# Kernel optimization log

Hardware: AMD Instinct MI355X
Metric: run time of the kernel (lower is better)

The kernel has to match this reference:

```python
import jax, jax.numpy as jnp
import numpy as np
from jax import lax

D_MODEL = 1024
D_STATE = 16
D_CONV = 4
EXPAND = 2
D_INNER = EXPAND * D_MODEL
LN_EPS = 1e-5


def setup_inputs() -> dict:
    key = jax.random.key(0)
    ks = jax.random.split(key, 12)
    B, L = 4, 1024
    s = lambda fan_in: 1.0 / np.sqrt(fan_in)
    inp = {
        "x": jax.random.normal(ks[0], (B, L, D_MODEL), jnp.float32),
        # in_proj: d_model -> 2*d_inner (stored as (in, out))
        "W_in": jax.random.normal(ks[1], (D_MODEL, 2 * D_INNER), jnp.float32) * s(D_MODEL),
        "b_in": jnp.zeros((2 * D_INNER,), jnp.float32),
        # depthwise causal conv1d, kernel (d_inner, 1, d_conv)
        "conv_w": jax.random.normal(ks[2], (D_INNER, 1, D_CONV), jnp.float32) * s(D_CONV),
        "conv_b": jnp.zeros((D_INNER,), jnp.float32),
        # x_proj: d_inner -> 2*d_state
        "W_xp": jax.random.normal(ks[3], (D_INNER, 2 * D_STATE), jnp.float32) * s(D_INNER),
        "b_xp": jnp.zeros((2 * D_STATE,), jnp.float32),
        # dt_proj: d_inner -> d_inner
        "W_dt": jax.random.normal(ks[4], (D_INNER, D_INNER), jnp.float32) * s(D_INNER),
        "b_dt": jnp.zeros((D_INNER,), jnp.float32),
        # A_log = log(arange(1, d_state+1)) repeated over d_inner
        "A_log": jnp.log(jnp.broadcast_to(jnp.arange(1, D_STATE + 1, dtype=jnp.float32), (D_INNER, D_STATE))),
        "D_param": jnp.ones((D_INNER,), jnp.float32),
        # out_proj: d_inner -> d_model
        "W_out": jax.random.normal(ks[5], (D_INNER, D_MODEL), jnp.float32) * s(D_INNER),
        "b_out": jnp.zeros((D_MODEL,), jnp.float32),
        "ln_g": jnp.ones((D_MODEL,), jnp.float32),
        "ln_b": jnp.zeros((D_MODEL,), jnp.float32),
    }
    return inp


def _causal_depthwise_conv(x, w, b):
    # x: (B, d_inner, L); w: (d_inner, 1, d_conv). Left-pad d_conv-1 => causal.
    y = lax.conv_general_dilated(
        x, w, window_strides=(1,), padding=[(D_CONV - 1, 0)],
        dimension_numbers=("NCH", "OIH", "NCH"), feature_group_count=D_INNER)
    return y + b[None, :, None]


def _ssm(x, A, Bm, Cm, dt, D_param):
    # x, dt: (B,L,D)  A: (D,N)  Bm, Cm: (B,L,N)
    A_disc = jnp.exp(dt[..., None] * A)               # (B,L,D,N)
    dBx = (dt * x)[..., None] * Bm[:, :, None, :]     # (B,L,D,N) = dt*B*x_t
    h0 = jnp.zeros(x.shape[:1] + A.shape, x.dtype)    # (B,D,N)

    def step(h, inputs):
        a, bx, c = inputs                              # (B,D,N),(B,D,N),(B,N)
        h = a * h + bx
        y = jnp.einsum("bdn,bn->bd", h, c)
        return h, y

    _, ys = lax.scan(step, h0, (jnp.swapaxes(A_disc, 0, 1),
                                jnp.swapaxes(dBx, 0, 1),
                                jnp.swapaxes(Cm, 0, 1)))
    y = jnp.swapaxes(ys, 0, 1)                         # (B,L,D)
    return y + x * D_param


def reference(x, W_in, b_in, conv_w, conv_b, W_xp, b_xp, W_dt, b_dt,
              A_log, D_param, W_out, b_out, ln_g, ln_b):
    residual = x
    xr = x @ W_in + b_in                               # (B,L,2*d_inner)
    xi, res = jnp.split(xr, 2, axis=-1)
    xi = jax.nn.silu(xi)
    xi = jnp.swapaxes(xi, 1, 2)                        # (B,d_inner,L)
    xi = _causal_depthwise_conv(xi, conv_w, conv_b)
    xi = jnp.swapaxes(xi, 1, 2)
    xi = jax.nn.silu(xi)
    bc = xi @ W_xp + b_xp                              # (B,L,2*d_state)
    Bm, Cm = jnp.split(bc, 2, axis=-1)
    dt = jax.nn.softplus(xi @ W_dt + b_dt)
    A = -jnp.exp(A_log)                                # (d_inner, d_state)
    y = _ssm(xi, A, Bm, Cm, dt, D_param)
    y = y * jax.nn.silu(res)
    out = y @ W_out + b_out
    z = out + residual
    mu = jnp.mean(z, axis=-1, keepdims=True)
    var = jnp.var(z, axis=-1, keepdims=True)
    return (z - mu) * jax.lax.rsqrt(var + LN_EPS) * ln_g + ln_b
```

## Files before the change

kernel.cpp:

```cpp
#include <hip/hip_runtime.h>
#include <math.h>

#define D_MODEL 1024
#define D_INNER 2048
#define D_STATE 16
#define D_CONV  4
#define NCHUNK  32
#define LCHUNK  32

typedef unsigned short u16;
typedef __attribute__((ext_vector_type(8))) short short8;
typedef __attribute__((ext_vector_type(4))) float f32x4;
typedef __attribute__((ext_vector_type(4))) unsigned short u16x4;
typedef __attribute__((ext_vector_type(8))) unsigned short u16x8;

__device__ __forceinline__ float silu_f(float x) { return x / (1.f + __expf(-x)); }
__device__ __forceinline__ float softplus_f(float x) {
    return fmaxf(x, 0.f) + log1pf(__expf(-fabsf(x)));
}
__device__ __forceinline__ u16 f2bf(float f) {
    union { float f; unsigned u; } c; c.f = f;
    unsigned r = c.u + 0x7fffu + ((c.u >> 16) & 1u);
    return (u16)(r >> 16);
}
__device__ __forceinline__ float bf2f(u16 v) {
    union { unsigned u; float f; } c; c.u = ((unsigned)v) << 16; return c.f;
}
__device__ __forceinline__ void gload_lds16(const void* g, void* l) {
    __builtin_amdgcn_global_load_lds((const __attribute__((address_space(1))) void*)g,
                                     (__attribute__((address_space(3))) void*)l, 16, 0, 0);
}

__global__ __launch_bounds__(256)
void f32_to_bf16_kernel(const float* __restrict__ in, u16* __restrict__ out, int n4)
{
    const int i = blockIdx.x * 256 + threadIdx.x;
    if (i >= n4) return;
    const float4 v = *(const float4*)&in[(size_t)i * 4];
    u16x4 o; o.x = f2bf(v.x); o.y = f2bf(v.y); o.z = f2bf(v.z); o.w = f2bf(v.w);
    *(u16x4*)&out[(size_t)i * 4] = o;
}

__global__ __launch_bounds__(256)
void transpose_bf16_kernel(const float* __restrict__ W, u16* __restrict__ Wt, int K, int N)
{
    __shared__ float tile[32][33];
    const int tx = threadIdx.x & 31, ty = threadIdx.x >> 5;
    const int n0 = blockIdx.x * 32, k0 = blockIdx.y * 32;
#pragma unroll
    for (int q = 0; q < 4; q++)
        tile[ty + q * 8][tx] = W[(size_t)(k0 + ty + q * 8) * N + n0 + tx];
    __syncthreads();
#pragma unroll
    for (int q = 0; q < 4; q++)
        Wt[(size_t)(n0 + ty + q * 8) * K + k0 + tx] = f2bf(tile[tx][ty + q * 8]);
}

template <int MODE>
__global__ __launch_bounds__(512, 2)
void gemm_mfma256(const u16* __restrict__ A, const u16* __restrict__ Bt,
                  const float* __restrict__ bias,
                  void* __restrict__ out0v, void* __restrict__ out1v,
                  int M, int N, int K)
{
    __shared__ __align__(16) short As[2][256 * 64];
    __shared__ __align__(16) short Bs[2][256 * 64];

    const int tid = threadIdx.x;
    const int wid = tid >> 6, lane = tid & 63;
    const int wr = wid >> 2, wc = wid & 3;
    const int row0 = blockIdx.y * 256, col0 = blockIdx.x * 256;
    const int kg = lane >> 4, r16 = lane & 15;

    f32x4 acc[8][4] = {};

    const u16* Abase = A + (size_t)row0 * K;
    const u16* Bbase = Bt + (size_t)col0 * K;

#define STAGE_A(bi, kk) do {                                                    \
        _Pragma("unroll")                                                       \
        for (int q = 0; q < 4; q++) {                                           \
            const int c = (q << 9) + tid;                                       \
            const int r = c >> 3;                                               \
            const int ks8 = (((c & 7) ^ (r & 7)) << 3);                         \
            gload_lds16(Abase + (size_t)r * K + (kk) + ks8,                     \
                        &As[bi][((q << 9) + (wid << 6)) << 3]);                 \
        }                                                                       \
    } while (0)
#define STAGE_B(bi, kk) do {                                                    \
        _Pragma("unroll")                                                       \
        for (int q = 0; q < 4; q++) {                                           \
            const int c = (q << 9) + tid;                                       \
            const int r = c >> 3;                                               \
            const int ks8 = (((c & 7) ^ (r & 7)) << 3);                         \
            gload_lds16(Bbase + (size_t)r * K + (kk) + ks8,                     \
                        &Bs[bi][((q << 9) + (wid << 6)) << 3]);                 \
        }                                                                       \
    } while (0)

    const int nt = K >> 6;
    STAGE_A(0, 0);
    STAGE_B(0, 0);

    int cur = 0;
    const int rx = r16 & 7;
    for (int t = 0; t < nt; ++t) {
        if (t + 1 < nt) {
            STAGE_A(cur ^ 1, (t + 1) << 6);
            asm volatile("s_waitcnt vmcnt(4)" ::: "memory");
        } else {
            asm volatile("s_waitcnt vmcnt(0)" ::: "memory");
        }
        __builtin_amdgcn_s_barrier();

#pragma unroll
        for (int ks = 0; ks < 2; ks++) {
            const int sl8 = (((ks << 2) + kg) ^ rx) << 3;
            short8 af[8], bg[4];
#pragma unroll
            for (int i = 0; i < 8; i++) {
                const int r = wr * 128 + i * 16 + r16;
                af[i] = *(const short8*)&As[cur][r * 64 + sl8];
            }
#pragma unroll
            for (int j = 0; j < 4; j++) {
                const int r = wc * 64 + j * 16 + r16;
                bg[j] = *(const short8*)&Bs[cur][r * 64 + sl8];
            }
            __builtin_amdgcn_s_setprio(1);
#pragma unroll
            for (int i = 0; i < 8; i++)
#pragma unroll
                for (int j = 0; j < 4; j++)
                    acc[i][j] = __builtin_amdgcn_mfma_f32_16x16x32_bf16(af[i], bg[j], acc[i][j], 0, 0, 0);
            __builtin_amdgcn_s_setprio(0);
            if (ks == 0 && t + 1 < nt)
                STAGE_B(cur ^ 1, (t + 1) << 6);
        }

        asm volatile("s_waitcnt lgkmcnt(0)" ::: "memory");
        __builtin_amdgcn_s_barrier();
        cur ^= 1;
    }
#undef STAGE_A
#undef STAGE_B

#pragma unroll
    for (int i = 0; i < 8; i++) {
#pragma unroll
        for (int j = 0; j < 4; j++) {
#pragma unroll
            for (int r = 0; r < 4; r++) {
                const int row = row0 + wr * 128 + i * 16 + kg * 4 + r;
                const int col = col0 + wc * 64 + j * 16 + r16;
                float v = acc[i][j][r] + bias[col];
                if (MODE == 0) {
                    u16* o0 = (u16*)out0v; u16* o1 = (u16*)out1v;
                    if (col < D_INNER) o0[(size_t)row * D_INNER + col] = f2bf(silu_f(v));
                    else               o1[(size_t)row * D_INNER + (col - D_INNER)] = f2bf(v);
                } else {
                    ((float*)out0v)[(size_t)row * N + col] = softplus_f(v);
                }
            }
        }
    }
}

template <int MODE>
__global__ __launch_bounds__(256)
void gemm_mfma_128(const u16* __restrict__ A, const u16* __restrict__ Bt,
                   const float* __restrict__ bias, const float* __restrict__ aux,
                   float* __restrict__ out0, int M, int N, int K)
{
    __shared__ __align__(16) short As[3][4096];
    __shared__ __align__(16) short Bs[3][4096];

    const int tid = threadIdx.x;
    const int wid = tid >> 6, lane = tid & 63;
    const int wr = wid >> 1, wc = wid & 1;
    const int row0 = blockIdx.y * 128, col0 = blockIdx.x * 128;

    f32x4 acc[4][4] = {};

    const int c0 = wid * 128 + lane;
    const int c1 = c0 + 64;
    const u16* Abase = A + (size_t)row0 * K;
    const u16* Bbase = Bt + (size_t)col0 * K;

    const int gsl8 = (((lane & 3) ^ ((lane >> 3) & 3)) << 3);
    const int kg = lane >> 4, r16 = lane & 15;
    const int sl8 = ((kg ^ ((r16 >> 1) & 3)) << 3);

#define STAGE(bi, kk) do {                                                                   \
        gload_lds16(Abase + (size_t)(c0 >> 2) * K + (kk) + gsl8, &As[bi][wid * 1024]);       \
        gload_lds16(Abase + (size_t)(c1 >> 2) * K + (kk) + gsl8, &As[bi][wid * 1024 + 512]); \
        gload_lds16(Bbase + (size_t)(c0 >> 2) * K + (kk) + gsl8, &Bs[bi][wid * 1024]);       \
        gload_lds16(Bbase + (size_t)(c1 >> 2) * K + (kk) + gsl8, &Bs[bi][wid * 1024 + 512]); \
    } while (0)

    const int nt = K >> 5;
    STAGE(0, 0);
    STAGE(1, 32);
    int cs = 0;
    for (int t = 0; t < nt; ++t) {
        if (t + 2 < nt) {
            const int ss = (cs + 2 >= 3) ? cs - 1 : cs + 2;
            STAGE(ss, (t + 2) << 5);
            asm volatile("s_waitcnt vmcnt(8)" ::: "memory");
        } else if (t + 1 < nt) {
            asm volatile("s_waitcnt vmcnt(4)" ::: "memory");
        } else {
            asm volatile("s_waitcnt vmcnt(0)" ::: "memory");
        }
        __builtin_amdgcn_s_barrier();

        short8 af[4], bg[4];
#pragma unroll
        for (int i = 0; i < 4; i++) {
            const int r = wr * 64 + i * 16 + r16;
            af[i] = *(const short8*)&As[cs][r * 32 + sl8];
        }
#pragma unroll
        for (int j = 0; j < 4; j++) {
            const int r = wc * 64 + j * 16 + r16;
            bg[j] = *(const short8*)&Bs[cs][r * 32 + sl8];
        }
        __builtin_amdgcn_s_setprio(1);
#pragma unroll
        for (int i = 0; i < 4; i++)
#pragma unroll
            for (int j = 0; j < 4; j++)
                acc[i][j] = __builtin_amdgcn_mfma_f32_16x16x32_bf16(af[i], bg[j], acc[i][j], 0, 0, 0);
        __builtin_amdgcn_s_setprio(0);

        asm volatile("s_waitcnt lgkmcnt(0)" ::: "memory");
        __builtin_amdgcn_s_barrier();
        cs = (cs + 1 >= 3) ? 0 : cs + 1;
    }
#undef STAGE

#pragma unroll
    for (int i = 0; i < 4; i++) {
#pragma unroll
        for (int j = 0; j < 4; j++) {
#pragma unroll
            for (int r = 0; r < 4; r++) {
                const int row = row0 + wr * 64 + i * 16 + kg * 4 + r;
                const int col = col0 + wc * 64 + j * 16 + r16;
                float v = acc[i][j][r] + bias[col];
                if (MODE == 1) out0[(size_t)row * N + col] = softplus_f(v);
                else           out0[(size_t)row * N + col] = v + aux[(size_t)row * N + col];
            }
        }
    }
}

__global__ __launch_bounds__(256)
void conv_silu8_kernel(const u16* __restrict__ xi, const float* __restrict__ w,
                       const float* __restrict__ cb, u16* __restrict__ xcb, int total8)
{
    const int i = blockIdx.x * 256 + threadIdx.x;
    if (i >= total8) return;
    const size_t i8 = (size_t)i * 8;
    const int d8 = (int)(i8 & (D_INNER - 1));
    const int l = (int)((i8 >> 11) & 1023);

    float acc[8];
#pragma unroll
    for (int c = 0; c < 8; c++) acc[c] = cb[d8 + c];

    float4 wv[8];
#pragma unroll
    for (int c = 0; c < 8; c++) wv[c] = *(const float4*)&w[(d8 + c) * 4];

#pragma unroll
    for (int k = 0; k < D_CONV; k++) {
        if (l + k - (D_CONV - 1) >= 0) {
            const u16x8 v = *(const u16x8*)&xi[i8 + (size_t)(k - (D_CONV - 1)) * D_INNER];
            const float wk0 = ((const float*)&wv[0])[k];
#pragma unroll
            for (int c = 0; c < 8; c++) {
                const float wk = ((const float*)&wv[c])[k];
                acc[c] = fmaf(wk, bf2f(v[c]), acc[c]);
            }
            (void)wk0;
        }
    }
    u16x8 o;
#pragma unroll
    for (int c = 0; c < 8; c++) o[c] = f2bf(silu_f(acc[c]));
    *(u16x8*)&xcb[i8] = o;
}

__global__ __launch_bounds__(256)
void xproj_mfma_kernel(const u16* __restrict__ A, const u16* __restrict__ Wt,
                       const float* __restrict__ bxp, float* __restrict__ bc)
{
    const int wid = threadIdx.x >> 6, lane = threadIdx.x & 63;
    const int kg = lane >> 4, r16 = lane & 15;
    const int tok0 = blockIdx.x * 64 + wid * 16;

    f32x4 acc[2] = {};
#pragma unroll 4
    for (int k0 = 0; k0 < D_INNER; k0 += 32) {
        const short8 a  = *(const short8*)&A[(size_t)(tok0 + r16) * D_INNER + k0 + kg * 8];
        const short8 b0 = *(const short8*)&Wt[(size_t)r16 * D_INNER + k0 + kg * 8];
        const short8 b1 = *(const short8*)&Wt[(size_t)(16 + r16) * D_INNER + k0 + kg * 8];
        acc[0] = __builtin_amdgcn_mfma_f32_16x16x32_bf16(a, b0, acc[0], 0, 0, 0);
        acc[1] = __builtin_amdgcn_mfma_f32_16x16x32_bf16(a, b1, acc[1], 0, 0, 0);
    }
#pragma unroll
    for (int j = 0; j < 2; j++)
#pragma unroll
        for (int r = 0; r < 4; r++) {
            const int token = tok0 + kg * 4 + r;
            const int c = j * 16 + r16;
            bc[(size_t)token * 32 + c] = acc[j][r] + bxp[c];
        }
}

__global__ __launch_bounds__(256)
void ssm_s1_kernel(const u16* __restrict__ xcbf, const float* __restrict__ dt,
                   const float* __restrict__ bc, const float* __restrict__ A_log,
                   float* __restrict__ hend, float* __restrict__ dtsum)
{
    const int tid = threadIdx.x;
    const int d = blockIdx.x * 256 + tid;
    const int c = blockIdx.y;
    const int b = blockIdx.z;

    __shared__ float sB[LCHUNK][16];
    {
        if (tid < LCHUNK * 4) {
            const int row = tid >> 2, c4 = (tid & 3) << 2;
            *(float4*)&sB[row][c4] = *(const float4*)&bc[((size_t)(b * 1024 + c * LCHUNK + row)) * 32 + c4];
        }
    }

    float Aln[D_STATE];
#pragma unroll
    for (int q = 0; q < 4; q++) {
        const f32x4 a = *(const f32x4*)&A_log[(size_t)d * D_STATE + q * 4];
        Aln[q * 4 + 0] = -__expf(a.x); Aln[q * 4 + 1] = -__expf(a.y);
        Aln[q * 4 + 2] = -__expf(a.z); Aln[q * 4 + 3] = -__expf(a.w);
    }

    const size_t base = ((size_t)(b * 1024 + c * LCHUNK)) * D_INNER + d;
    const float* dtp = dt + base;
    const u16* xp = xcbf + base;

    float h[D_STATE] = {};
    float S = 0.f;
    __syncthreads();

#pragma unroll 16
    for (int j = 0; j < LCHUNK; j++) {
        const float dtf = dtp[(size_t)j * D_INNER];
        const float xf = bf2f(xp[(size_t)j * D_INNER]);
        const float dtx = dtf * xf;
        S += dtf;
#pragma unroll
        for (int n = 0; n < D_STATE; n++) {
            const float a = __expf(dtf * Aln[n]);
            h[n] = fmaf(a, h[n], dtx * sB[j][n]);
        }
    }

    const size_t ob = ((size_t)(b * NCHUNK + c) * D_INNER + d);
#pragma unroll
    for (int q = 0; q < 4; q++) {
        f32x4 hv = {h[q * 4 + 0], h[q * 4 + 1], h[q * 4 + 2], h[q * 4 + 3]};
        *(f32x4*)&hend[ob * D_STATE + q * 4] = hv;
    }
    dtsum[ob] = S;
}

__global__ __launch_bounds__(256)
void ssm_s2_kernel(const float* __restrict__ hend, const float* __restrict__ dtsum,
                   const float* __restrict__ A_log, float* __restrict__ hin)
{
    const int tid = threadIdx.x;
    const int d = blockIdx.x * 16 + (tid >> 4);
    const int n = tid & 15;
    const int b = blockIdx.y;

    const float Aln = -__expf(A_log[(size_t)d * D_STATE + n]);
    float h = 0.f;
#pragma unroll
    for (int c = 0; c < NCHUNK; c++) {
        const size_t ob = ((size_t)(b * NCHUNK + c) * D_INNER + d);
        hin[ob * D_STATE + n] = h;
        const float P = __expf(Aln * dtsum[ob]);
        h = fmaf(P, h, hend[ob * D_STATE + n]);
    }
}

__global__ __launch_bounds__(256)
void ssm_s3_kernel(const u16* __restrict__ xcbf, const float* __restrict__ dt,
                   const float* __restrict__ bc, const float* __restrict__ A_log,
                   const float* __restrict__ Dp, const u16* __restrict__ resbf,
                   const float* __restrict__ hin, u16* __restrict__ ybf)
{
    const int tid = threadIdx.x;
    const int d = blockIdx.x * 256 + tid;
    const int c = blockIdx.y;
    const int b = blockIdx.z;

    __shared__ float sbc[LCHUNK][32];
    {
        const int row = tid >> 3, c4 = (tid & 7) << 2;
        if (row < LCHUNK)
            *(float4*)&sbc[row][c4] = *(const float4*)&bc[((size_t)(b * 1024 + c * LCHUNK + row)) * 32 + c4];
    }

    float Aln[D_STATE];
#pragma unroll
    for (int q = 0; q < 4; q++) {
        const f32x4 a = *(const f32x4*)&A_log[(size_t)d * D_STATE + q * 4];
        Aln[q * 4 + 0] = -__expf(a.x); Aln[q * 4 + 1] = -__expf(a.y);
        Aln[q * 4 + 2] = -__expf(a.z); Aln[q * 4 + 3] = -__expf(a.w);
    }
    const float Dv = Dp[d];

    float h[D_STATE];
    const size_t ob = ((size_t)(b * NCHUNK + c) * D_INNER + d);
#pragma unroll
    for (int q = 0; q < 4; q++) {
        const f32x4 hv = *(const f32x4*)&hin[ob * D_STATE + q * 4];
        h[q * 4 + 0] = hv.x; h[q * 4 + 1] = hv.y; h[q * 4 + 2] = hv.z; h[q * 4 + 3] = hv.w;
    }

    const size_t base = ((size_t)(b * 1024 + c * LCHUNK)) * D_INNER + d;
    const float* dtp = dt + base;
    const u16* xp = xcbf + base;
    const u16* rp = resbf + base;
    u16* yp = ybf + base;

    __syncthreads();

#pragma unroll 16
    for (int j = 0; j < LCHUNK; j++) {
        const float dtf = dtp[(size_t)j * D_INNER];
        const float xf = bf2f(xp[(size_t)j * D_INNER]);
        const float rf = bf2f(rp[(size_t)j * D_INNER]);
        const float dtx = dtf * xf;
        float yv = 0.f;
#pragma unroll
        for (int n = 0; n < D_STATE; n++) {
            const float a = __expf(dtf * Aln[n]);
            h[n] = fmaf(a, h[n], dtx * sbc[j][n]);
            yv = fmaf(h[n], sbc[j][16 + n], yv);
        }
        yv = (yv + xf * Dv) * silu_f(rf);
        yp[(size_t)j * D_INNER] = f2bf(yv);
    }
}

__global__ __launch_bounds__(256)
void layernorm_kernel(const float* __restrict__ z, const float* __restrict__ g,
                      const float* __restrict__ beta, float* __restrict__ out)
{
    const int row = blockIdx.x;
    const int tid = threadIdx.x;
    const float* zr = z + (size_t)row * D_MODEL;
    const float4 v = *(const float4*)&zr[tid << 2];
    float s = v.x + v.y + v.z + v.w;
    float ss = v.x * v.x + v.y * v.y + v.z * v.z + v.w * v.w;

    __shared__ float sm[256], sq[256];
    sm[tid] = s; sq[tid] = ss;
    __syncthreads();
    for (int off = 128; off > 0; off >>= 1) {
        if (tid < off) { sm[tid] += sm[tid + off]; sq[tid] += sq[tid + off]; }
        __syncthreads();
    }
    const float mean = sm[0] * (1.f / D_MODEL);
    const float var = sq[0] * (1.f / D_MODEL) - mean * mean;
    const float rstd = rsqrtf(var + 1e-5f);

    float4 o;
    o.x = (v.x - mean) * rstd * g[(tid << 2) + 0] + beta[(tid << 2) + 0];
    o.y = (v.y - mean) * rstd * g[(tid << 2) + 1] + beta[(tid << 2) + 1];
    o.z = (v.z - mean) * rstd * g[(tid << 2) + 2] + beta[(tid << 2) + 2];
    o.w = (v.w - mean) * rstd * g[(tid << 2) + 3] + beta[(tid << 2) + 3];
    *(float4*)&out[(size_t)row * D_MODEL + (tid << 2)] = o;
}

extern "C" void kernel_launch(void* const* d_in, const int* in_sizes, int n_in,
                              void* d_out, int out_size, void* d_ws, size_t ws_size,
                              hipStream_t stream)
{
    const float* x      = (const float*)d_in[0];
    const float* W_in   = (const float*)d_in[1];
    const float* b_in   = (const float*)d_in[2];
    const float* conv_w = (const float*)d_in[3];
    const float* conv_b = (const float*)d_in[4];
    const float* W_xp   = (const float*)d_in[5];
    const float* b_xp   = (const float*)d_in[6];
    const float* W_dt   = (const float*)d_in[7];
    const float* b_dt   = (const float*)d_in[8];
    const float* A_log  = (const float*)d_in[9];
    const float* D_par  = (const float*)d_in[10];
    const float* W_out  = (const float*)d_in[11];
    const float* b_out  = (const float*)d_in[12];
    const float* ln_g   = (const float*)d_in[13];
    const float* ln_b   = (const float*)d_in[14];
    float* out = (float*)d_out;

    const int BL = in_sizes[0] / D_MODEL;
    const int Bb = BL / 1024;
    const size_t BLD = (size_t)BL * D_INNER;

    float* ws    = (float*)d_ws;
    float* dtb   = ws;
    float* bcbuf = dtb + BLD;
    float* hend  = bcbuf + (size_t)BL * 32;
    float* dtsum = hend + (size_t)Bb * NCHUNK * D_INNER * D_STATE;
    float* hinb  = dtsum + (size_t)Bb * NCHUNK * D_INNER;
    u16*   xibf  = (u16*)(hinb + (size_t)Bb * NCHUNK * D_INNER * D_STATE);
    u16*   resbf = xibf + BLD;
    u16*   xcbf  = resbf + BLD;
    u16*   xbf   = xcbf + BLD;
    u16*   wxpT  = xbf + (size_t)BL * D_MODEL;
    u16*   wtmp  = wxpT + 32 * D_INNER;
    u16*   ybf   = xibf;
    float* zbuf  = dtb;

    f32_to_bf16_kernel<<<(BL * D_MODEL / 4 + 255) / 256, 256, 0, stream>>>(x, xbf, BL * D_MODEL / 4);

    transpose_bf16_kernel<<<dim3(2 * D_INNER / 32, D_MODEL / 32), 256, 0, stream>>>(W_in, wtmp, D_MODEL, 2 * D_INNER);

    gemm_mfma256<0><<<dim3(2 * D_INNER / 256, BL / 256), 512, 0, stream>>>(
        xbf, wtmp, b_in, xibf, resbf, BL, 2 * D_INNER, D_MODEL);

    transpose_bf16_kernel<<<dim3(1, D_INNER / 32), 256, 0, stream>>>(W_xp, wxpT, D_INNER, 32);

    conv_silu8_kernel<<<(int)(BLD / 8 / 256), 256, 0, stream>>>(
        xibf, conv_w, conv_b, xcbf, (int)(BLD / 8));

    xproj_mfma_kernel<<<BL / 64, 256, 0, stream>>>(xcbf, wxpT, b_xp, bcbuf);

    transpose_bf16_kernel<<<dim3(D_INNER / 32, D_INNER / 32), 256, 0, stream>>>(W_dt, wtmp, D_INNER, D_INNER);

    gemm_mfma_128<1><<<dim3(D_INNER / 128, BL / 128), 256, 0, stream>>>(
        xcbf, wtmp, b_dt, nullptr, dtb, BL, D_INNER, D_INNER);

    ssm_s1_kernel<<<dim3(D_INNER / 256, NCHUNK, Bb), 256, 0, stream>>>(
        xcbf, dtb, bcbuf, A_log, hend, dtsum);

    ssm_s2_kernel<<<dim3(D_INNER / 16, Bb), 256, 0, stream>>>(
        hend, dtsum, A_log, hinb);

    ssm_s3_kernel<<<dim3(D_INNER / 256, NCHUNK, Bb), 256, 0, stream>>>(
        xcbf, dtb, bcbuf, A_log, D_par, resbf, hinb, ybf);

    transpose_bf16_kernel<<<dim3(D_MODEL / 32, D_INNER / 32), 256, 0, stream>>>(W_out, wtmp, D_INNER, D_MODEL);

    gemm_mfma_128<2><<<dim3(D_MODEL / 128, BL / 128), 256, 0, stream>>>(
        ybf, wtmp, b_out, x, zbuf, BL, D_MODEL, D_INNER);

    layernorm_kernel<<<BL, 256, 0, stream>>>(zbuf, ln_g, ln_b, out);
}
```

Before: 327.9 us.

## Store dt as bf16 and add a 256x128 double-buffered dt-projection GEMM

Replaces the 128x128 GEMM for the dt projection with a new 512-thread, 256x128-tile kernel. It uses an XOR-swizzled double-buffered LDS layout, staggers A and B prefetches around the MFMA work, and writes softplus(dt) as bf16 instead of fp32. Both SSM scan kernels now read dt as bf16, which halves dt traffic on the write and on both read passes. The workspace is relaid out so the out-projection result reuses the chunk-state buffer. The cost is reduced dt precision feeding the exponentials in the recurrence.

```diff
diff --git a/kernel.cpp b/kernel.cpp
--- a/kernel.cpp
+++ b/kernel.cpp
@@ -166,7 +166,108 @@
     }
 }
 
-template <int MODE>
+__global__ __launch_bounds__(512, 2)
+void gemm_dt256(const u16* __restrict__ A, const u16* __restrict__ Bt,
+                const float* __restrict__ bias, u16* __restrict__ out0,
+                int M, int N, int K)
+{
+    __shared__ __align__(16) short As[2][256 * 64];
+    __shared__ __align__(16) short Bs[2][128 * 64];
+
+    const int tid = threadIdx.x;
+    const int wid = tid >> 6, lane = tid & 63;
+    const int wr = wid >> 1, wc = wid & 1;
+    const int row0 = blockIdx.y * 256, col0 = blockIdx.x * 128;
+    const int kg = lane >> 4, r16 = lane & 15;
+
+    f32x4 acc[4][4] = {};
+
+    const u16* Abase = A + (size_t)row0 * K;
+    const u16* Bbase = Bt + (size_t)col0 * K;
+
+#define STAGE_A(bi, kk) do {                                                    \
+        _Pragma("unroll")                                                       \
+        for (int q = 0; q < 4; q++) {                                           \
+            const int c = (q << 9) + tid;                                       \
+            const int r = c >> 3;                                               \
+            const int ks8 = (((c & 7) ^ (r & 7)) << 3);                         \
+            gload_lds16(Abase + (size_t)r * K + (kk) + ks8,                     \
+                        &As[bi][((q << 9) + (wid << 6)) << 3]);                 \
+        }                                                                       \
+    } while (0)
+#define STAGE_B(bi, kk) do {                                                    \
+        _Pragma("unroll")                                                       \
+        for (int q = 0; q < 2; q++) {                                           \
+            const int c = (q << 9) + tid;                                       \
+            const int r = c >> 3;                                               \
+            const int ks8 = (((c & 7) ^ (r & 7)) << 3);                         \
+            gload_lds16(Bbase + (size_t)r * K + (kk) + ks8,                     \
+                        &Bs[bi][((q << 9) + (wid << 6)) << 3]);                 \
+        }                                                                       \
+    } while (0)
+
+    const int nt = K >> 6;
+    STAGE_A(0, 0);
+    STAGE_B(0, 0);
+
+    int cur = 0;
+    const int rx = r16 & 7;
+    for (int t = 0; t < nt; ++t) {
+        if (t + 1 < nt) {
+            STAGE_A(cur ^ 1, (t + 1) << 6);
+            asm volatile("s_waitcnt vmcnt(4)" ::: "memory");
+        } else {
+            asm volatile("s_waitcnt vmcnt(0)" ::: "memory");
+        }
+        __builtin_amdgcn_s_barrier();
+
+#pragma unroll
+        for (int ks = 0; ks < 2; ks++) {
+            const int sl8 = (((ks << 2) + kg) ^ rx) << 3;
+            short8 af[4], bg[4];
+#pragma unroll
+            for (int i = 0; i < 4; i++) {
+                const int r = wr * 64 + i * 16 + r16;
+                af[i] = *(const short8*)&As[cur][r * 64 + sl8];
+            }
+#pragma unroll
+            for (int j = 0; j < 4; j++) {
+                const int r = wc * 64 + j * 16 + r16;
+                bg[j] = *(const short8*)&Bs[cur][r * 64 + sl8];
+            }
+            __builtin_amdgcn_s_setprio(1);
+#pragma unroll
+            for (int i = 0; i < 4; i++)
+#pragma unroll
+                for (int j = 0; j < 4; j++)
+                    acc[i][j] = __builtin_amdgcn_mfma_f32_16x16x32_bf16(af[i], bg[j], acc[i][j], 0, 0, 0);
+            __builtin_amdgcn_s_setprio(0);
+            if (ks == 0 && t + 1 < nt)
+                STAGE_B(cur ^ 1, (t + 1) << 6);
+        }
+
+        asm volatile("s_waitcnt lgkmcnt(0)" ::: "memory");
+        __builtin_amdgcn_s_barrier();
+        cur ^= 1;
+    }
+#undef STAGE_A
+#undef STAGE_B
+
+#pragma unroll
+    for (int i = 0; i < 4; i++) {
+#pragma unroll
+        for (int j = 0; j < 4; j++) {
+#pragma unroll
+            for (int r = 0; r < 4; r++) {
+                const int row = row0 + wr * 64 + i * 16 + kg * 4 + r;
+                const int col = col0 + wc * 64 + j * 16 + r16;
+                const float v = acc[i][j][r] + bias[col];
+                out0[(size_t)row * N + col] = f2bf(softplus_f(v));
+            }
+        }
+    }
+}
+
 __global__ __launch_bounds__(256)
 void gemm_mfma_128(const u16* __restrict__ A, const u16* __restrict__ Bt,
                    const float* __restrict__ bias, const float* __restrict__ aux,
@@ -247,9 +348,8 @@
             for (int r = 0; r < 4; r++) {
                 const int row = row0 + wr * 64 + i * 16 + kg * 4 + r;
                 const int col = col0 + wc * 64 + j * 16 + r16;
-                float v = acc[i][j][r] + bias[col];
-                if (MODE == 1) out0[(size_t)row * N + col] = softplus_f(v);
-                else           out0[(size_t)row * N + col] = v + aux[(size_t)row * N + col];
+                const float v = acc[i][j][r] + bias[col];
+                out0[(size_t)row * N + col] = v + aux[(size_t)row * N + col];
             }
         }
     }
@@ -277,13 +377,11 @@
     for (int k = 0; k < D_CONV; k++) {
         if (l + k - (D_CONV - 1) >= 0) {
             const u16x8 v = *(const u16x8*)&xi[i8 + (size_t)(k - (D_CONV - 1)) * D_INNER];
-            const float wk0 = ((const float*)&wv[0])[k];
 #pragma unroll
             for (int c = 0; c < 8; c++) {
                 const float wk = ((const float*)&wv[c])[k];
                 acc[c] = fmaf(wk, bf2f(v[c]), acc[c]);
             }
-            (void)wk0;
         }
     }
     u16x8 o;
@@ -320,7 +418,7 @@
 }
 
 __global__ __launch_bounds__(256)
-void ssm_s1_kernel(const u16* __restrict__ xcbf, const float* __restrict__ dt,
+void ssm_s1_kernel(const u16* __restrict__ xcbf, const u16* __restrict__ dtbf,
                    const float* __restrict__ bc, const float* __restrict__ A_log,
                    float* __restrict__ hend, float* __restrict__ dtsum)
 {
@@ -346,7 +444,7 @@
     }
 
     const size_t base = ((size_t)(b * 1024 + c * LCHUNK)) * D_INNER + d;
-    const float* dtp = dt + base;
+    const u16* dtp = dtbf + base;
     const u16* xp = xcbf + base;
 
     float h[D_STATE] = {};
@@ -355,7 +453,7 @@
 
 #pragma unroll 16
     for (int j = 0; j < LCHUNK; j++) {
-        const float dtf = dtp[(size_t)j * D_INNER];
+        const float dtf = bf2f(dtp[(size_t)j * D_INNER]);
         const float xf = bf2f(xp[(size_t)j * D_INNER]);
         const float dtx = dtf * xf;
         S += dtf;
@@ -396,7 +494,7 @@
 }
 
 __global__ __launch_bounds__(256)
-void ssm_s3_kernel(const u16* __restrict__ xcbf, const float* __restrict__ dt,
+void ssm_s3_kernel(const u16* __restrict__ xcbf, const u16* __restrict__ dtbf,
                    const float* __restrict__ bc, const float* __restrict__ A_log,
                    const float* __restrict__ Dp, const u16* __restrict__ resbf,
                    const float* __restrict__ hin, u16* __restrict__ ybf)
@@ -431,7 +529,7 @@
     }
 
     const size_t base = ((size_t)(b * 1024 + c * LCHUNK)) * D_INNER + d;
-    const float* dtp = dt + base;
+    const u16* dtp = dtbf + base;
     const u16* xp = xcbf + base;
     const u16* rp = resbf + base;
     u16* yp = ybf + base;
@@ -440,7 +538,7 @@
 
 #pragma unroll 16
     for (int j = 0; j < LCHUNK; j++) {
-        const float dtf = dtp[(size_t)j * D_INNER];
+        const float dtf = bf2f(dtp[(size_t)j * D_INNER]);
         const float xf = bf2f(xp[(size_t)j * D_INNER]);
         const float rf = bf2f(rp[(size_t)j * D_INNER]);
         const float dtx = dtf * xf;
@@ -512,19 +610,19 @@
     const size_t BLD = (size_t)BL * D_INNER;
 
     float* ws    = (float*)d_ws;
-    float* dtb   = ws;
-    float* bcbuf = dtb + BLD;
+    float* bcbuf = ws;
     float* hend  = bcbuf + (size_t)BL * 32;
     float* dtsum = hend + (size_t)Bb * NCHUNK * D_INNER * D_STATE;
     float* hinb  = dtsum + (size_t)Bb * NCHUNK * D_INNER;
     u16*   xibf  = (u16*)(hinb + (size_t)Bb * NCHUNK * D_INNER * D_STATE);
     u16*   resbf = xibf + BLD;
     u16*   xcbf  = resbf + BLD;
-    u16*   xbf   = xcbf + BLD;
+    u16*   dtbf  = xcbf + BLD;
+    u16*   xbf   = dtbf + BLD;
     u16*   wxpT  = xbf + (size_t)BL * D_MODEL;
     u16*   wtmp  = wxpT + 32 * D_INNER;
     u16*   ybf   = xibf;
-    float* zbuf  = dtb;
+    float* zbuf  = hend;
 
     f32_to_bf16_kernel<<<(BL * D_MODEL / 4 + 255) / 256, 256, 0, stream>>>(x, xbf, BL * D_MODEL / 4);
 
@@ -542,21 +640,21 @@
 
     transpose_bf16_kernel<<<dim3(D_INNER / 32, D_INNER / 32), 256, 0, stream>>>(W_dt, wtmp, D_INNER, D_INNER);
 
-    gemm_mfma_128<1><<<dim3(D_INNER / 128, BL / 128), 256, 0, stream>>>(
-        xcbf, wtmp, b_dt, nullptr, dtb, BL, D_INNER, D_INNER);
+    gemm_dt256<<<dim3(D_INNER / 128, BL / 256), 512, 0, stream>>>(
+        xcbf, wtmp, b_dt, dtbf, BL, D_INNER, D_INNER);
 
     ssm_s1_kernel<<<dim3(D_INNER / 256, NCHUNK, Bb), 256, 0, stream>>>(
-        xcbf, dtb, bcbuf, A_log, hend, dtsum);
+        xcbf, dtbf, bcbuf, A_log, hend, dtsum);
 
     ssm_s2_kernel<<<dim3(D_INNER / 16, Bb), 256, 0, stream>>>(
         hend, dtsum, A_log, hinb);
 
     ssm_s3_kernel<<<dim3(D_INNER / 256, NCHUNK, Bb), 256, 0, stream>>>(
-        xcbf, dtb, bcbuf, A_log, D_par, resbf, hinb, ybf);
+        xcbf, dtbf, bcbuf, A_log, D_par, resbf, hinb, ybf);
 
     transpose_bf16_kernel<<<dim3(D_MODEL / 32, D_INNER / 32), 256, 0, stream>>>(W_out, wtmp, D_INNER, D_MODEL);
 
-    gemm_mfma_128<2><<<dim3(D_MODEL / 128, BL / 128), 256, 0, stream>>>(
+    gemm_mfma_128<<<dim3(D_MODEL / 128, BL / 128), 256, 0, stream>>>(
         ybf, wtmp, b_out, x, zbuf, BL, D_MODEL, D_INNER);
 
     layernorm_kernel<<<BL, 256, 0, stream>>>(zbuf, ln_g, ln_b, out);
```

Result: no change. 333.6 us (+1.7%).

## Rewrite 256x256 GEMM as 8-phase pipelined kernel and store dt in bf16

Applied to the files above, without the earlier changes.

Replaces the double-buffered 256x256 GEMM with an 8-phase schedule. Each K-tile pair is split into quarter-tile MFMA groups with barriers between them, A/B half-tile staging is interleaved with the groups, and workgroups are remapped for L2 locality. The dt_proj GEMM now uses this 256-tile kernel and writes softplus(dt) as bf16, so the SSM kernels read half the bytes. Risks are extra barrier overhead, 1 wave-group per CU occupancy, and reduced dt precision in the scan.

```diff
diff --git a/kernel.cpp b/kernel.cpp
--- a/kernel.cpp
+++ b/kernel.cpp
@@ -57,93 +57,133 @@
 }
 
 template <int MODE>
-__global__ __launch_bounds__(512, 2)
-void gemm_mfma256(const u16* __restrict__ A, const u16* __restrict__ Bt,
-                  const float* __restrict__ bias,
-                  void* __restrict__ out0v, void* __restrict__ out1v,
-                  int M, int N, int K)
-{
-    __shared__ __align__(16) short As[2][256 * 64];
-    __shared__ __align__(16) short Bs[2][256 * 64];
+__global__ __launch_bounds__(512, 1)
+void gemm_8ph(const u16* __restrict__ A, const u16* __restrict__ Bt,
+              const float* __restrict__ bias,
+              void* __restrict__ out0v, void* __restrict__ out1v,
+              int M, int N, int K)
+{
+    __shared__ __align__(16) short As[2][16384];
+    __shared__ __align__(16) short Bs[2][16384];
 
     const int tid = threadIdx.x;
     const int wid = tid >> 6, lane = tid & 63;
     const int wr = wid >> 2, wc = wid & 3;
-    const int row0 = blockIdx.y * 256, col0 = blockIdx.x * 256;
     const int kg = lane >> 4, r16 = lane & 15;
+    const int rx = r16 & 7;
+
+    int lb = blockIdx.y * gridDim.x + blockIdx.x;
+    const int nwg = gridDim.x * gridDim.y;
+    lb = (lb & 7) * (nwg >> 3) + (lb >> 3);
+    const int bx = lb % gridDim.x, by = lb / gridDim.x;
+    const int row0 = by * 256, col0 = bx * 256;
 
     f32x4 acc[8][4] = {};
-
     const u16* Abase = A + (size_t)row0 * K;
     const u16* Bbase = Bt + (size_t)col0 * K;
 
-#define STAGE_A(bi, kk) do {                                                    \
+#define STAGE_AH(bi, mh, kk) do {                                               \
         _Pragma("unroll")                                                       \
-        for (int q = 0; q < 4; q++) {                                           \
+        for (int q = 0; q < 2; q++) {                                           \
             const int c = (q << 9) + tid;                                       \
-            const int r = c >> 3;                                               \
-            const int ks8 = (((c & 7) ^ (r & 7)) << 3);                         \
-            gload_lds16(Abase + (size_t)r * K + (kk) + ks8,                     \
-                        &As[bi][((q << 9) + (wid << 6)) << 3]);                 \
+            const int rr = c >> 3;                                              \
+            const int ks8 = (((c & 7) ^ (rr & 7)) << 3);                        \
+            gload_lds16(Abase + (size_t)((mh) * 128 + rr) * K + (kk) + ks8,     \
+                        &As[bi][(((mh) << 10) + (q << 9) + (wid << 6)) << 3]);  \
         }                                                                       \
     } while (0)
-#define STAGE_B(bi, kk) do {                                                    \
+#define STAGE_BH(bi, mh, kk) do {                                               \
         _Pragma("unroll")                                                       \
-        for (int q = 0; q < 4; q++) {                                           \
+        for (int q = 0; q < 2; q++) {                                           \
             const int c = (q << 9) + tid;                                       \
-            const int r = c >> 3;                                               \
-            const int ks8 = (((c & 7) ^ (r & 7)) << 3);                         \
-            gload_lds16(Bbase + (size_t)r * K + (kk) + ks8,                     \
-                        &Bs[bi][((q << 9) + (wid << 6)) << 3]);                 \
+            const int rr = c >> 3;                                              \
+            const int ks8 = (((c & 7) ^ (rr & 7)) << 3);                        \
+            gload_lds16(Bbase + (size_t)((mh) * 128 + rr) * K + (kk) + ks8,     \
+                        &Bs[bi][(((mh) << 10) + (q << 9) + (wid << 6)) << 3]);  \
         }                                                                       \
     } while (0)
-
-    const int nt = K >> 6;
-    STAGE_A(0, 0);
-    STAGE_B(0, 0);
-
-    int cur = 0;
-    const int rx = r16 & 7;
-    for (int t = 0; t < nt; ++t) {
-        if (t + 1 < nt) {
-            STAGE_A(cur ^ 1, (t + 1) << 6);
-            asm volatile("s_waitcnt vmcnt(4)" ::: "memory");
-        } else {
-            asm volatile("s_waitcnt vmcnt(0)" ::: "memory");
-        }
-        __builtin_amdgcn_s_barrier();
-
-#pragma unroll
-        for (int ks = 0; ks < 2; ks++) {
-            const int sl8 = (((ks << 2) + kg) ^ rx) << 3;
-            short8 af[8], bg[4];
-#pragma unroll
-            for (int i = 0; i < 8; i++) {
-                const int r = wr * 128 + i * 16 + r16;
-                af[i] = *(const short8*)&As[cur][r * 64 + sl8];
-            }
-#pragma unroll
-            for (int j = 0; j < 4; j++) {
-                const int r = wc * 64 + j * 16 + r16;
-                bg[j] = *(const short8*)&Bs[cur][r * 64 + sl8];
-            }
-            __builtin_amdgcn_s_setprio(1);
-#pragma unroll
-            for (int i = 0; i < 8; i++)
-#pragma unroll
-                for (int j = 0; j < 4; j++)
-                    acc[i][j] = __builtin_amdgcn_mfma_f32_16x16x32_bf16(af[i], bg[j], acc[i][j], 0, 0, 0);
-            __builtin_amdgcn_s_setprio(0);
-            if (ks == 0 && t + 1 < nt)
-                STAGE_B(cur ^ 1, (t + 1) << 6);
-        }
-
-        asm volatile("s_waitcnt lgkmcnt(0)" ::: "memory");
-        __builtin_amdgcn_s_barrier();
-        cur ^= 1;
-    }
-#undef STAGE_A
-#undef STAGE_B
+#define LOAD_AF(bi, mh) do {                                                    \
+        _Pragma("unroll")                                                       \
+        for (int ii = 0; ii < 4; ii++) {                                        \
+            const int rr = wr * 128 + (mh) * 64 + ii * 16 + r16;                \
+            af[0][ii] = *(const short8*)&As[bi][rr * 64 + ((kg ^ rx) << 3)];    \
+            af[1][ii] = *(const short8*)&As[bi][rr * 64 + (((4 + kg) ^ rx) << 3)]; \
+        }                                                                       \
+    } while (0)
+#define LOAD_BG(bi, nh) do {                                                    \
+        _Pragma("unroll")                                                       \
+        for (int jj = 0; jj < 2; jj++) {                                        \
+            const int rr = wc * 64 + (nh) * 32 + jj * 16 + r16;                 \
+            bg[0][jj] = *(const short8*)&Bs[bi][rr * 64 + ((kg ^ rx) << 3)];    \
+            bg[1][jj] = *(const short8*)&Bs[bi][rr * 64 + (((4 + kg) ^ rx) << 3)]; \
+        }                                                                       \
+    } while (0)
+#define QUAD(nh, mh) do {                                                       \
+        _Pragma("unroll")                                                       \
+        for (int ks = 0; ks < 2; ks++)                                          \
+            _Pragma("unroll")                                                   \
+            for (int ii = 0; ii < 4; ii++)                                      \
+                _Pragma("unroll")                                               \
+                for (int jj = 0; jj < 2; jj++)                                  \
+                    acc[(mh) * 4 + ii][(nh) * 2 + jj] =                         \
+                        __builtin_amdgcn_mfma_f32_16x16x32_bf16(                \
+                            af[ks][ii], bg[ks][jj],                             \
+                            acc[(mh) * 4 + ii][(nh) * 2 + jj], 0, 0, 0);        \
+    } while (0)
+#define PH_SYNC do { __builtin_amdgcn_s_barrier();                              \
+        asm volatile("s_waitcnt lgkmcnt(0)" ::: "memory"); } while (0)
+#define PRIO1 __builtin_amdgcn_s_setprio(1)
+#define PRIO0 __builtin_amdgcn_s_setprio(0)
+#define ENDBAR __builtin_amdgcn_s_barrier()
+#define VMC4 asm volatile("s_waitcnt vmcnt(4)" ::: "memory")
+
+    const int ntile = K >> 6;
+    STAGE_AH(0, 0, 0); STAGE_AH(0, 1, 0);
+    STAGE_BH(0, 0, 0); STAGE_BH(0, 1, 0);
+    STAGE_BH(1, 0, 64); STAGE_BH(1, 1, 64);
+    VMC4;
+    __builtin_amdgcn_s_barrier();
+
+    short8 af[2][4], bg[2][2];
+    for (int T = 0; T < ntile; T += 2) {
+        const int kA1 = (T + 1) << 6;
+        const int kN2 = ((T + 2) & (ntile - 1)) << 6;
+        const int kN3 = ((T + 3) & (ntile - 1)) << 6;
+        LOAD_AF(0, 0); LOAD_BG(0, 0);
+        STAGE_AH(1, 0, kA1);
+        PH_SYNC; PRIO1; QUAD(0, 0); PRIO0; ENDBAR;
+        LOAD_AF(0, 1);
+        STAGE_AH(1, 1, kA1);
+        PH_SYNC; PRIO1; QUAD(0, 1); PRIO0; ENDBAR;
+        LOAD_BG(0, 1);
+        PH_SYNC; PRIO1; QUAD(1, 1); PRIO0; ENDBAR;
+        LOAD_AF(0, 0);
+        STAGE_BH(0, 0, kN2); STAGE_BH(0, 1, kN2);
+        VMC4;
+        PH_SYNC; PRIO1; QUAD(1, 0); PRIO0; ENDBAR;
+        LOAD_AF(1, 0); LOAD_BG(1, 0);
+        STAGE_AH(0, 0, kN2);
+        PH_SYNC; PRIO1; QUAD(0, 0); PRIO0; ENDBAR;
+        LOAD_AF(1, 1);
+        STAGE_AH(0, 1, kN2);
+        PH_SYNC; PRIO1; QUAD(0, 1); PRIO0; ENDBAR;
+        LOAD_BG(1, 1);
+        PH_SYNC; PRIO1; QUAD(1, 1); PRIO0; ENDBAR;
+        LOAD_AF(1, 0);
+        STAGE_BH(1, 0, kN3); STAGE_BH(1, 1, kN3);
+        VMC4;
+        PH_SYNC; PRIO1; QUAD(1, 0); PRIO0; ENDBAR;
+    }
+#undef STAGE_AH
+#undef STAGE_BH
+#undef LOAD_AF
+#undef LOAD_BG
+#undef QUAD
+#undef PH_SYNC
+#undef PRIO1
+#undef PRIO0
+#undef ENDBAR
+#undef VMC4
 
 #pragma unroll
     for (int i = 0; i < 8; i++) {
@@ -153,20 +193,19 @@
             for (int r = 0; r < 4; r++) {
                 const int row = row0 + wr * 128 + i * 16 + kg * 4 + r;
                 const int col = col0 + wc * 64 + j * 16 + r16;
-                float v = acc[i][j][r] + bias[col];
+                const float v = acc[i][j][r] + bias[col];
                 if (MODE == 0) {
                     u16* o0 = (u16*)out0v; u16* o1 = (u16*)out1v;
                     if (col < D_INNER) o0[(size_t)row * D_INNER + col] = f2bf(silu_f(v));
                     else               o1[(size_t)row * D_INNER + (col - D_INNER)] = f2bf(v);
                 } else {
-                    ((float*)out0v)[(size_t)row * N + col] = softplus_f(v);
+                    ((u16*)out0v)[(size_t)row * N + col] = f2bf(softplus_f(v));
                 }
             }
         }
     }
 }
 
-template <int MODE>
 __global__ __launch_bounds__(256)
 void gemm_mfma_128(const u16* __restrict__ A, const u16* __restrict__ Bt,
                    const float* __restrict__ bias, const float* __restrict__ aux,
@@ -247,9 +286,8 @@
             for (int r = 0; r < 4; r++) {
                 const int row = row0 + wr * 64 + i * 16 + kg * 4 + r;
                 const int col = col0 + wc * 64 + j * 16 + r16;
-                float v = acc[i][j][r] + bias[col];
-                if (MODE == 1) out0[(size_t)row * N + col] = softplus_f(v);
-                else           out0[(size_t)row * N + col] = v + aux[(size_t)row * N + col];
+                const float v = acc[i][j][r] + bias[col];
+                out0[(size_t)row * N + col] = v + aux[(size_t)row * N + col];
             }
         }
     }
@@ -277,13 +315,11 @@
     for (int k = 0; k < D_CONV; k++) {
         if (l + k - (D_CONV - 1) >= 0) {
             const u16x8 v = *(const u16x8*)&xi[i8 + (size_t)(k - (D_CONV - 1)) * D_INNER];
-            const float wk0 = ((const float*)&wv[0])[k];
 #pragma unroll
             for (int c = 0; c < 8; c++) {
                 const float wk = ((const float*)&wv[c])[k];
                 acc[c] = fmaf(wk, bf2f(v[c]), acc[c]);
             }
-            (void)wk0;
         }
     }
     u16x8 o;
@@ -320,7 +356,7 @@
 }
 
 __global__ __launch_bounds__(256)
-void ssm_s1_kernel(const u16* __restrict__ xcbf, const float* __restrict__ dt,
+void ssm_s1_kernel(const u16* __restrict__ xcbf, const u16* __restrict__ dtbf,
                    const float* __restrict__ bc, const float* __restrict__ A_log,
                    float* __restrict__ hend, float* __restrict__ dtsum)
 {
@@ -346,7 +382,7 @@
     }
 
     const size_t base = ((size_t)(b * 1024 + c * LCHUNK)) * D_INNER + d;
-    const float* dtp = dt + base;
+    const u16* dtp = dtbf + base;
     const u16* xp = xcbf + base;
 
     float h[D_STATE] = {};
@@ -355,7 +391,7 @@
 
 #pragma unroll 16
     for (int j = 0; j < LCHUNK; j++) {
-        const float dtf = dtp[(size_t)j * D_INNER];
+        const float dtf = bf2f(dtp[(size_t)j * D_INNER]);
         const float xf = bf2f(xp[(size_t)j * D_INNER]);
         const float dtx = dtf * xf;
         S += dtf;
@@ -396,7 +432,7 @@
 }
 
 __global__ __launch_bounds__(256)
-void ssm_s3_kernel(const u16* __restrict__ xcbf, const float* __restrict__ dt,
+void ssm_s3_kernel(const u16* __restrict__ xcbf, const u16* __restrict__ dtbf,
                    const float* __restrict__ bc, const float* __restrict__ A_log,
                    const float* __restrict__ Dp, const u16* __restrict__ resbf,
                    const float* __restrict__ hin, u16* __restrict__ ybf)
@@ -431,7 +467,7 @@
     }
 
     const size_t base = ((size_t)(b * 1024 + c * LCHUNK)) * D_INNER + d;
-    const float* dtp = dt + base;
+    const u16* dtp = dtbf + base;
     const u16* xp = xcbf + base;
     const u16* rp = resbf + base;
     u16* yp = ybf + base;
@@ -440,7 +476,7 @@
 
 #pragma unroll 16
     for (int j = 0; j < LCHUNK; j++) {
-        const float dtf = dtp[(size_t)j * D_INNER];
+        const float dtf = bf2f(dtp[(size_t)j * D_INNER]);
         const float xf = bf2f(xp[(size_t)j * D_INNER]);
         const float rf = bf2f(rp[(size_t)j * D_INNER]);
         const float dtx = dtf * xf;
@@ -512,25 +548,25 @@
     const size_t BLD = (size_t)BL * D_INNER;
 
     float* ws    = (float*)d_ws;
-    float* dtb   = ws;
-    float* bcbuf = dtb + BLD;
+    float* bcbuf = ws;
     float* hend  = bcbuf + (size_t)BL * 32;
     float* dtsum = hend + (size_t)Bb * NCHUNK * D_INNER * D_STATE;
     float* hinb  = dtsum + (size_t)Bb * NCHUNK * D_INNER;
     u16*   xibf  = (u16*)(hinb + (size_t)Bb * NCHUNK * D_INNER * D_STATE);
     u16*   resbf = xibf + BLD;
     u16*   xcbf  = resbf + BLD;
-    u16*   xbf   = xcbf + BLD;
+    u16*   dtbf  = xcbf + BLD;
+    u16*   xbf   = dtbf + BLD;
     u16*   wxpT  = xbf + (size_t)BL * D_MODEL;
     u16*   wtmp  = wxpT + 32 * D_INNER;
     u16*   ybf   = xibf;
-    float* zbuf  = dtb;
+    float* zbuf  = hend;
 
     f32_to_bf16_kernel<<<(BL * D_MODEL / 4 + 255) / 256, 256, 0, stream>>>(x, xbf, BL * D_MODEL / 4);
 
     transpose_bf16_kernel<<<dim3(2 * D_INNER / 32, D_MODEL / 32), 256, 0, stream>>>(W_in, wtmp, D_MODEL, 2 * D_INNER);
 
-    gemm_mfma256<0><<<dim3(2 * D_INNER / 256, BL / 256), 512, 0, stream>>>(
+    gemm_8ph<0><<<dim3(2 * D_INNER / 256, BL / 256), 512, 0, stream>>>(
         xbf, wtmp, b_in, xibf, resbf, BL, 2 * D_INNER, D_MODEL);
 
     transpose_bf16_kernel<<<dim3(1, D_INNER / 32), 256, 0, stream>>>(W_xp, wxpT, D_INNER, 32);
@@ -542,21 +578,21 @@
 
     transpose_bf16_kernel<<<dim3(D_INNER / 32, D_INNER / 32), 256, 0, stream>>>(W_dt, wtmp, D_INNER, D_INNER);
 
-    gemm_mfma_128<1><<<dim3(D_INNER / 128, BL / 128), 256, 0, stream>>>(
-        xcbf, wtmp, b_dt, nullptr, dtb, BL, D_INNER, D_INNER);
+    gemm_8ph<1><<<dim3(D_INNER / 256, BL / 256), 512, 0, stream>>>(
+        xcbf, wtmp, b_dt, dtbf, nullptr, BL, D_INNER, D_INNER);
 
     ssm_s1_kernel<<<dim3(D_INNER / 256, NCHUNK, Bb), 256, 0, stream>>>(
-        xcbf, dtb, bcbuf, A_log, hend, dtsum);
+        xcbf, dtbf, bcbuf, A_log, hend, dtsum);
 
     ssm_s2_kernel<<<dim3(D_INNER / 16, Bb), 256, 0, stream>>>(
         hend, dtsum, A_log, hinb);
 
     ssm_s3_kernel<<<dim3(D_INNER / 256, NCHUNK, Bb), 256, 0, stream>>>(
-        xcbf, dtb, bcbuf, A_log, D_par, resbf, hinb, ybf);
+        xcbf, dtbf, bcbuf, A_log, D_par, resbf, hinb, ybf);
 
     transpose_bf16_kernel<<<dim3(D_MODEL / 32, D_INNER / 32), 256, 0, stream>>>(W_out, wtmp, D_INNER, D_MODEL);
 
-    gemm_mfma_128<2><<<dim3(D_MODEL / 128, BL / 128), 256, 0, stream>>>(
+    gemm_mfma_128<<<dim3(D_MODEL / 128, BL / 128), 256, 0, stream>>>(
         ybf, wtmp, b_out, x, zbuf, BL, D_MODEL, D_INNER);
 
     layernorm_kernel<<<BL, 256, 0, stream>>>(zbuf, ln_g, ln_b, out);
```

After: 813.1 us. +148.0%, slower.
